# Kernel tuning notes

Measured on AMD Instinct MI355X. Metric: run time of the kernel, lower is better.

## Reference

```python
import jax, jax.numpy as jnp
import numpy as np

B, S, H = 8, 2048, 1024

def setup_inputs() -> dict:
    key = jax.random.key(0)
    k1, k2, k3, k4, k5, k6 = jax.random.split(key, 6)
    scale = 1.0 / np.sqrt(H)
    return {
        "hidden_states": jax.random.normal(k1, (B, S, H), dtype=jnp.float32),
        "key_padding_mask": jax.random.bernoulli(k2, 0.1, (B, S)),  # True = padded key
        "Wq_w": jax.random.normal(k3, (H, H), dtype=jnp.float32) * scale,
        "Wq_b": jax.random.normal(k4, (H,), dtype=jnp.float32) * 0.01,
        "Wk_w": jax.random.normal(k5, (H, H), dtype=jnp.float32) * scale,
        "Wk_b": jax.random.normal(k6, (H,), dtype=jnp.float32) * 0.01,
    }

def reference(hidden_states, key_padding_mask, Wq_w, Wq_b, Wk_w, Wk_b):
    # torch nn.Linear: y = x @ W.T + b
    q = jnp.einsum("bsh,oh->bso", hidden_states, Wq_w) + Wq_b
    k = jnp.einsum("bsh,oh->bso", hidden_states, Wk_w) + Wk_b
    d = q.shape[-1]
    scores = jnp.einsum("bqd,bkd->bqk", q, k) / jnp.sqrt(jnp.asarray(d, q.dtype))
    # scores[mask] -= inf  -> masked key columns become -inf
    scores = jnp.where(key_padding_mask[:, None, :], -jnp.inf, scores)
    attn = jax.nn.softmax(scores, axis=2)  # [B, S, S]
    out = jnp.einsum("bqk,bkd->bqd", attn, hidden_states)  # values = hidden_states (no proj)
    return out
```

## Files before the change

kernel.cpp:

```cpp
#include <hip/hip_runtime.h>
#include <hip/hip_bf16.h>

using bf16 = __hip_bfloat16;

using frag_ab = __attribute__((ext_vector_type(8))) short;
using frag_cd = __attribute__((ext_vector_type(4))) float;

__device__ __forceinline__ unsigned short f2bu(float f) {
    bf16 h = __float2bfloat16(f);
    return *(unsigned short*)&h;
}

__device__ __forceinline__ void st_c(float* p, float v) { *p = v; }
__device__ __forceinline__ void st_c(bf16* p, float v)  { *p = __float2bfloat16(v); }

__device__ __forceinline__ void load16(const bf16* g, bf16* l) {
    __builtin_amdgcn_global_load_lds(
        (const __attribute__((address_space(1))) unsigned int*)g,
        (__attribute__((address_space(3))) unsigned int*)l,
        16, 0, 0);
}

template <typename TC, bool HAS_BIAS, bool MASK>
__global__ __launch_bounds__(512, 2)
void gemm8p(const bf16* __restrict__ A, const bf16* __restrict__ B,
            const float* __restrict__ bias, const int* __restrict__ mask,
            TC* __restrict__ C, int K, int lda, int ldb, int ldc,
            long sA, long sB, long sC, long sM, float scale)
{
    __shared__ short lds[65536];

    const int bz = blockIdx.z;
    const bf16* Ab = A + (long)bz * sA;
    const bf16* Bb = B + (long)bz * sB;
    TC* Cb = C + (long)bz * sC;
    const int* maskb = MASK ? (mask + (long)bz * sM) : nullptr;

    const int t    = threadIdx.x;
    const int wid  = t >> 6;
    const int lane = t & 63;
    const int m0 = blockIdx.x * 256;
    const int n0 = blockIdx.y * 256;
    const int wr = wid >> 2;
    const int wc = wid & 3;
    const int lrow = lane & 15;
    const int quad = lane >> 4;

    const int rco   = ((quad + ((lrow >> 1) & 3)) & 3) * 8;
    const int a_off = wr * 4096 + lrow * 32 + rco;
    const int b_off = wc * 2048 + lrow * 32 + rco;

    const int srow = wid * 32 + (lane >> 2);
    const int gk   = (((lane & 3) - (lane >> 3)) & 3) * 8;
    const bf16* srcA0 = Ab + (long)(m0 + srow) * lda + gk;
    const bf16* srcA1 = Ab + (long)(m0 + srow + 16) * lda + gk;
    const bf16* srcB0 = Bb + (long)(n0 + srow) * ldb + gk;
    const bf16* srcB1 = Bb + (long)(n0 + srow + 16) * ldb + gk;
    const int dst0 = wid * 1024 + lane * 8;

    frag_cd acc[8][4] = {};
    frag_ab A0[4], A1[4], B0[4], B1[4];

#define STG(SLOT, PART, K0)                                                     \
    do {                                                                        \
        load16((PART ? srcB0 : srcA0) + (K0),                                   \
               (bf16*)&lds[(SLOT) * 16384 + (PART) * 8192 + dst0]);             \
        load16((PART ? srcB1 : srcA1) + (K0),                                   \
               (bf16*)&lds[(SLOT) * 16384 + (PART) * 8192 + dst0 + 512]);       \
    } while (0)

#define LOADA(DST, SLOT, QM)                                                    \
    do {                                                                        \
        _Pragma("unroll")                                                       \
        for (int i_ = 0; i_ < 4; ++i_)                                          \
            DST[i_] = *(const frag_ab*)&lds[(SLOT) * 16384 + a_off +            \
                                            (QM) * 2048 + i_ * 512];            \
    } while (0)

#define LOADB(DST, SLOT)                                                        \
    do {                                                                        \
        _Pragma("unroll")                                                       \
        for (int j_ = 0; j_ < 4; ++j_)                                          \
            DST[j_] = *(const frag_ab*)&lds[(SLOT) * 16384 + 8192 + b_off +     \
                                            j_ * 512];                          \
    } while (0)

#define MFMA16(AR, BR, QM)                                                      \
    do {                                                                        \
        _Pragma("unroll")                                                       \
        for (int i_ = 0; i_ < 4; ++i_)                                          \
            _Pragma("unroll")                                                   \
            for (int j_ = 0; j_ < 4; ++j_)                                      \
                acc[(QM) * 4 + i_][j_] = __builtin_amdgcn_mfma_f32_16x16x32_bf16( \
                    AR[i_], BR[j_], acc[(QM) * 4 + i_][j_], 0, 0, 0);           \
    } while (0)

#define VMW(N)                                                                  \
    do {                                                                        \
        if ((N) == 6)      asm volatile("s_waitcnt vmcnt(6)" ::: "memory");     \
        else if ((N) == 4) asm volatile("s_waitcnt vmcnt(4)" ::: "memory");     \
        else if ((N) == 0) asm volatile("s_waitcnt vmcnt(0)" ::: "memory");     \
    } while (0)

#define PH(AR, BR, QM, ISSUE, NSLOT, NAR, NBR, NQM, DO_STG, SSLOT, SPART, SK0, VMN) \
    do {                                                                        \
        if ((ISSUE) >= 1) LOADA(NAR, NSLOT, NQM);                               \
        if ((ISSUE) == 2) LOADB(NBR, NSLOT);                                    \
        if (DO_STG) STG(SSLOT, SPART, SK0);                                     \
        asm volatile("" ::: "memory");                                          \
        __builtin_amdgcn_s_setprio(1);                                          \
        MFMA16(AR, BR, QM);                                                     \
        __builtin_amdgcn_s_setprio(0);                                          \
        VMW(VMN);                                                               \
        asm volatile("" ::: "memory");                                          \
        __builtin_amdgcn_s_barrier();                                           \
        asm volatile("" ::: "memory");                                          \
    } while (0)

    STG(0, 0, 0);  STG(0, 1, 0);
    STG(1, 0, 32); STG(1, 1, 32);
    STG(2, 0, 64); STG(2, 1, 64);
    asm volatile("s_waitcnt vmcnt(8)" ::: "memory");
    __builtin_amdgcn_s_barrier();
    asm volatile("" ::: "memory");
    LOADA(A0, 0, 0);
    LOADB(B0, 0);

    const int NI = K >> 7;
    for (int it = 0; it < NI - 1; ++it) {
        const int kb = it << 7;
        PH(A0, B0, 0, 1, 0, A1, B1, 1, 1, 3, 0, kb + 96,   6);
        PH(A1, B0, 1, 2, 1, A0, B1, 0, 1, 3, 1, kb + 96,  -1);
        PH(A0, B1, 0, 1, 1, A1, B0, 1, 1, 0, 0, kb + 128,  6);
        PH(A1, B1, 1, 2, 2, A0, B0, 0, 1, 0, 1, kb + 128, -1);
        PH(A0, B0, 0, 1, 2, A1, B1, 1, 1, 1, 0, kb + 160,  6);
        PH(A1, B0, 1, 2, 3, A0, B1, 0, 1, 1, 1, kb + 160, -1);
        PH(A0, B1, 0, 1, 3, A1, B0, 1, 1, 2, 0, kb + 192,  6);
        PH(A1, B1, 1, 2, 0, A0, B0, 0, 1, 2, 1, kb + 192, -1);
    }
    {
        const int kb = (NI - 1) << 7;
        PH(A0, B0, 0, 1, 0, A1, B1, 1, 1, 3, 0, kb + 96,   6);
        PH(A1, B0, 1, 2, 1, A0, B1, 0, 1, 3, 1, kb + 96,  -1);
        PH(A0, B1, 0, 1, 1, A1, B0, 1, 0, 0, 0, 0,         4);
        PH(A1, B1, 1, 2, 2, A0, B0, 0, 0, 0, 0, 0,        -1);
        PH(A0, B0, 0, 1, 2, A1, B1, 1, 0, 0, 0, 0,         0);
        PH(A1, B0, 1, 2, 3, A0, B1, 0, 0, 0, 0, 0,        -1);
        PH(A0, B1, 0, 1, 3, A1, B0, 1, 0, 0, 0, 0,        -1);
        PH(A1, B1, 1, 0, 0, A0, B0, 0, 0, 0, 0, 0,        -1);
    }
#undef PH
#undef VMW
#undef MFMA16
#undef LOADB
#undef LOADA
#undef STG

#pragma unroll
    for (int j = 0; j < 4; ++j) {
        const int col = n0 + wc * 64 + j * 16 + lrow;
        const float bv = HAS_BIAS ? bias[col] : 0.0f;
        const bool msk = MASK ? (maskb[col] != 0) : false;
#pragma unroll
        for (int ai = 0; ai < 8; ++ai) {
            const int rbase = m0 + wr * 128 + ai * 16 + quad * 4;
#pragma unroll
            for (int r = 0; r < 4; ++r) {
                float v = acc[ai][j][r] * scale + bv;
                if (MASK && msk) v = -INFINITY;
                st_c(&Cb[(long)(rbase + r) * ldc + col], v);
            }
        }
    }
}

__global__ __launch_bounds__(256)
void convert_transpose(const float* __restrict__ X, bf16* __restrict__ Xb,
                       bf16* __restrict__ XT, int S, int H)
{
    __shared__ unsigned short tile[64][72];
    const int b = blockIdx.z;
    const float* Xp = X + (long)b * S * H;
    bf16* Xbp = Xb + (long)b * S * H;
    bf16* XTp = XT + (long)b * H * S;
    const int h0 = blockIdx.x * 64, s0 = blockIdx.y * 64;
    const int t = threadIdx.x;
    const int r  = t >> 4;
    const int c4 = (t & 15) * 4;

#pragma unroll
    for (int p = 0; p < 4; ++p) {
        const int row = r + p * 16;
        const float4 v = *(const float4*)&Xp[(long)(s0 + row) * H + h0 + c4];
        ushort4 u;
        u.x = f2bu(v.x); u.y = f2bu(v.y); u.z = f2bu(v.z); u.w = f2bu(v.w);
        *(ushort4*)&tile[row][c4] = u;
        *(ushort4*)&Xbp[(long)(s0 + row) * H + h0 + c4] = u;
    }
    __syncthreads();
#pragma unroll
    for (int p = 0; p < 4; ++p) {
        const int hrow = r + p * 16;
        ushort4 u;
        u.x = tile[c4 + 0][hrow];
        u.y = tile[c4 + 1][hrow];
        u.z = tile[c4 + 2][hrow];
        u.w = tile[c4 + 3][hrow];
        *(ushort4*)&XTp[(long)(h0 + hrow) * S + s0 + c4] = u;
    }
}

__global__ __launch_bounds__(256)
void convert_w2(const float* __restrict__ wa, const float* __restrict__ wb,
                bf16* __restrict__ out, int n4each)
{
    const int i = blockIdx.x * 256 + threadIdx.x;
    const bool second = i >= n4each;
    const float* src = second ? wb : wa;
    const int j = second ? i - n4each : i;
    const float4 v = ((const float4*)src)[j];
    ushort4 u;
    u.x = f2bu(v.x); u.y = f2bu(v.y); u.z = f2bu(v.z); u.w = f2bu(v.w);
    ((ushort4*)out)[i] = u;
}

__global__ __launch_bounds__(256)
void pack_bias(const float* __restrict__ qb, const float* __restrict__ kb,
               float* __restrict__ out, int H)
{
    const int i = blockIdx.x * 256 + threadIdx.x;
    out[i] = (i < H) ? qb[i] : kb[i - H];
}

__global__ __launch_bounds__(256)
void softmax_kernel(bf16* __restrict__ Smat, int Slen)
{
    const int row = blockIdx.x;
    bf16* srow = Smat + (long)row * Slen;

    const int t    = threadIdx.x;
    const int lane = t & 63;
    const int wid  = t >> 6;

    ushort4 u0 = ((const ushort4*)srow)[t * 2];
    ushort4 u1 = ((const ushort4*)srow)[t * 2 + 1];

    float vals[8];
    {
        const unsigned short us[8] = {u0.x, u0.y, u0.z, u0.w, u1.x, u1.y, u1.z, u1.w};
#pragma unroll
        for (int i = 0; i < 8; ++i) {
            unsigned int w = (unsigned int)us[i] << 16;
            vals[i] = *(float*)&w;
        }
    }

    float mx = vals[0];
#pragma unroll
    for (int i = 1; i < 8; ++i) mx = fmaxf(mx, vals[i]);

    __shared__ float red[4];
#pragma unroll
    for (int o = 32; o > 0; o >>= 1) mx = fmaxf(mx, __shfl_xor(mx, o, 64));
    if (lane == 0) red[wid] = mx;
    __syncthreads();
    mx = fmaxf(fmaxf(red[0], red[1]), fmaxf(red[2], red[3]));
    __syncthreads();

    float sum = 0.0f;
#pragma unroll
    for (int i = 0; i < 8; ++i) {
        const float e = __expf(vals[i] - mx);
        vals[i] = e;
        sum += e;
    }
#pragma unroll
    for (int o = 32; o > 0; o >>= 1) sum += __shfl_xor(sum, o, 64);
    if (lane == 0) red[wid] = sum;
    __syncthreads();
    sum = red[0] + red[1] + red[2] + red[3];

    const float inv = 1.0f / sum;
    ushort4 o0, o1;
    o0.x = f2bu(vals[0] * inv); o0.y = f2bu(vals[1] * inv);
    o0.z = f2bu(vals[2] * inv); o0.w = f2bu(vals[3] * inv);
    o1.x = f2bu(vals[4] * inv); o1.y = f2bu(vals[5] * inv);
    o1.z = f2bu(vals[6] * inv); o1.w = f2bu(vals[7] * inv);
    ((ushort4*)srow)[t * 2]     = o0;
    ((ushort4*)srow)[t * 2 + 1] = o1;
}

extern "C" void kernel_launch(void* const* d_in, const int* in_sizes, int n_in,
                              void* d_out, int out_size, void* d_ws, size_t ws_size,
                              hipStream_t stream)
{
    const float* hidden = (const float*)d_in[0];
    const int*   mask   = (const int*)d_in[1];
    const float* Wq_w   = (const float*)d_in[2];
    const float* Wq_b   = (const float*)d_in[3];
    const float* Wk_w   = (const float*)d_in[4];
    const float* Wk_b   = (const float*)d_in[5];
    float* out = (float*)d_out;

    const int B = 8, S = 2048, H = 1024;
    const int M = B * S;
    const long MH = (long)M * H;

    bf16* QK  = (bf16*)d_ws;
    bf16* XbT = QK + MH * 2;
    bf16* Sb  = XbT + MH;
    bf16* Xb  = Sb;
    bf16* Wb  = Xb + MH;
    float* biasP = (float*)(Wb + 2L * H * H);

    const dim3 blk(256);
    const dim3 blk512(512);

    convert_transpose<<<dim3(H / 64, S / 64, B), blk, 0, stream>>>(hidden, Xb, XbT, S, H);
    convert_w2<<<dim3(2 * H * H / 1024), blk, 0, stream>>>(Wq_w, Wk_w, Wb, H * H / 4);
    pack_bias<<<dim3(2 * H / 256), blk, 0, stream>>>(Wq_b, Wk_b, biasP, H);

    gemm8p<bf16, true, false><<<dim3(M / 256, 2 * H / 256, 1), blk512, 0, stream>>>(
        Xb, Wb, biasP, nullptr, QK, H, H, H, 2 * H, 0, 0, 0, 0, 1.0f);

    gemm8p<bf16, false, true><<<dim3(S / 256, S / 256, B), blk512, 0, stream>>>(
        QK, QK + H, nullptr, mask, Sb, H, 2 * H, 2 * H, S,
        (long)S * 2 * H, (long)S * 2 * H, (long)S * S, S, 1.0f / 32.0f);

    softmax_kernel<<<dim3(B * S), blk, 0, stream>>>(Sb, S);

    gemm8p<float, false, false><<<dim3(S / 256, H / 256, B), blk512, 0, stream>>>(
        Sb, XbT, nullptr, nullptr, out, S, S, S, H,
        (long)S * S, (long)H * S, (long)S * H, 0, 1.0f);
}
```

Measured before the change: 383.0 us.

## Fold Q and K projections into a single precomputed Wq^T Wk product

Uses the identity QK^T = X(Wq^T Wk)X^T + terms that are constant per row, which softmax cancels. The only term kept is a per-key bias X·(Wk^T bq), computed by a row-dot kernel. The combined weight matrix is built once per call by a small MFMA GEMM. This replaces the 2H-wide projection GEMM with one H-wide GEMM, and the scores GEMM now reads T and X directly. The cost is extra transposes and helper kernels, plus possible bf16 rounding differences from the reassociated product.

```diff
diff --git a/kernel.cpp b/kernel.cpp
--- a/kernel.cpp
+++ b/kernel.cpp
@@ -5,10 +5,18 @@
 
 using frag_ab = __attribute__((ext_vector_type(8))) short;
 using frag_cd = __attribute__((ext_vector_type(4))) float;
+
+#define TM 128
+#define TN 128
+#define TK 32
 
 __device__ __forceinline__ unsigned short f2bu(float f) {
     bf16 h = __float2bfloat16(f);
     return *(unsigned short*)&h;
+}
+__device__ __forceinline__ float bu2f(unsigned short u) {
+    unsigned int w = (unsigned int)u << 16;
+    return *(float*)&w;
 }
 
 __device__ __forceinline__ void st_c(float* p, float v) { *p = v; }
@@ -26,7 +34,7 @@
 void gemm8p(const bf16* __restrict__ A, const bf16* __restrict__ B,
             const float* __restrict__ bias, const int* __restrict__ mask,
             TC* __restrict__ C, int K, int lda, int ldb, int ldc,
-            long sA, long sB, long sC, long sM, float scale)
+            long sA, long sB, long sC, long sM, long sBias, float scale)
 {
     __shared__ short lds[65536];
 
@@ -35,6 +43,7 @@
     const bf16* Bb = B + (long)bz * sB;
     TC* Cb = C + (long)bz * sC;
     const int* maskb = MASK ? (mask + (long)bz * sM) : nullptr;
+    const float* biasb = HAS_BIAS ? (bias + (long)bz * sBias) : nullptr;
 
     const int t    = threadIdx.x;
     const int wid  = t >> 6;
@@ -159,14 +168,106 @@
 #pragma unroll
     for (int j = 0; j < 4; ++j) {
         const int col = n0 + wc * 64 + j * 16 + lrow;
+        const float bv = HAS_BIAS ? biasb[col] : 0.0f;
+        const bool msk = MASK ? (maskb[col] != 0) : false;
+#pragma unroll
+        for (int ai = 0; ai < 8; ++ai) {
+            const int rbase = m0 + wr * 128 + ai * 16 + quad * 4;
+#pragma unroll
+            for (int r = 0; r < 4; ++r) {
+                float v = acc[ai][j][r] * scale + bv;
+                if (MASK && msk) v = -INFINITY;
+                st_c(&Cb[(long)(rbase + r) * ldc + col], v);
+            }
+        }
+    }
+}
+
+template <typename TC, bool HAS_BIAS, bool MASK>
+__global__ __launch_bounds__(256, 4)
+void mfma_gemm_nt(const bf16* __restrict__ A, const bf16* __restrict__ B,
+                  const float* __restrict__ bias, const int* __restrict__ mask,
+                  TC* __restrict__ C, int N, int K, int lda, int ldb, int ldc,
+                  long sA, long sB, long sC, long sM, float scale)
+{
+    __shared__ bf16 As[2][TM][TK];
+    __shared__ bf16 Bs[2][TN][TK];
+
+    const int bz = blockIdx.z;
+    const bf16* Ab = A + (long)bz * sA;
+    const bf16* Bb = B + (long)bz * sB;
+    TC* Cb = C + (long)bz * sC;
+    const int* maskb = MASK ? (mask + (long)bz * sM) : nullptr;
+
+    const int t  = threadIdx.x;
+    const int m0 = blockIdx.x * TM;
+    const int n0 = blockIdx.y * TN;
+
+    const int srow = t >> 2;
+    const int c    = t & 3;
+    const int gco  = (((c - (srow >> 1)) & 3) << 3);
+    const int lco  = c << 3;
+    const bf16* ga0 = Ab + (long)(m0 + srow) * lda + gco;
+    const bf16* ga1 = ga0 + (long)64 * lda;
+    const bf16* gb0 = Bb + (long)(n0 + srow) * ldb + gco;
+    const bf16* gb1 = gb0 + (long)64 * ldb;
+
+    const int wave = t >> 6;
+    const int lane = t & 63;
+    const int wm   = (wave & 1) * 64;
+    const int wn   = (wave >> 1) * 64;
+    const int lrow = lane & 15;
+    const int quad = lane >> 4;
+    const int rco  = (((quad + (lrow >> 1)) & 3) << 3);
+
+    frag_cd acc[4][4] = {};
+
+#define STAGE(buf)                                         \
+    do {                                                   \
+        load16(ga0, &As[buf][srow][lco]);                  \
+        load16(ga1, &As[buf][srow + 64][lco]);             \
+        load16(gb0, &Bs[buf][srow][lco]);                  \
+        load16(gb1, &Bs[buf][srow + 64][lco]);             \
+        ga0 += TK; ga1 += TK; gb0 += TK; gb1 += TK;        \
+    } while (0)
+
+    STAGE(0);
+    __syncthreads();
+
+    int cur = 0;
+    for (int k0 = 0; k0 < K; k0 += TK) {
+        if (k0 + TK < K) STAGE(cur ^ 1);
+
+        frag_ab af[4], bfv[4];
+#pragma unroll
+        for (int i = 0; i < 4; ++i)
+            af[i] = *(const frag_ab*)&As[cur][wm + i * 16 + lrow][rco];
+#pragma unroll
+        for (int j = 0; j < 4; ++j)
+            bfv[j] = *(const frag_ab*)&Bs[cur][wn + j * 16 + lrow][rco];
+#pragma unroll
+        for (int i = 0; i < 4; ++i)
+#pragma unroll
+            for (int j = 0; j < 4; ++j)
+                acc[i][j] = __builtin_amdgcn_mfma_f32_16x16x32_bf16(
+                    af[i], bfv[j], acc[i][j], 0, 0, 0);
+
+        __syncthreads();
+        cur ^= 1;
+    }
+#undef STAGE
+
+#pragma unroll
+    for (int j = 0; j < 4; ++j) {
+        const int col = n0 + wn + j * 16 + lrow;
         const float bv = HAS_BIAS ? bias[col] : 0.0f;
         const bool msk = MASK ? (maskb[col] != 0) : false;
 #pragma unroll
-        for (int ai = 0; ai < 8; ++ai) {
-            const int rbase = m0 + wr * 128 + ai * 16 + quad * 4;
+        for (int i = 0; i < 4; ++i) {
+            const int rbase = m0 + wm + i * 16 + quad * 4;
 #pragma unroll
             for (int r = 0; r < 4; ++r) {
-                float v = acc[ai][j][r] * scale + bv;
+                float v = acc[i][j][r] * scale + bv;
                 if (MASK && msk) v = -INFINITY;
                 st_c(&Cb[(long)(rbase + r) * ldc + col], v);
             }
@@ -211,25 +312,25 @@
 }
 
 __global__ __launch_bounds__(256)
-void convert_w2(const float* __restrict__ wa, const float* __restrict__ wb,
-                bf16* __restrict__ out, int n4each)
-{
-    const int i = blockIdx.x * 256 + threadIdx.x;
-    const bool second = i >= n4each;
-    const float* src = second ? wb : wa;
-    const int j = second ? i - n4each : i;
-    const float4 v = ((const float4*)src)[j];
-    ushort4 u;
-    u.x = f2bu(v.x); u.y = f2bu(v.y); u.z = f2bu(v.z); u.w = f2bu(v.w);
-    ((ushort4*)out)[i] = u;
-}
-
-__global__ __launch_bounds__(256)
-void pack_bias(const float* __restrict__ qb, const float* __restrict__ kb,
-               float* __restrict__ out, int H)
-{
-    const int i = blockIdx.x * 256 + threadIdx.x;
-    out[i] = (i < H) ? qb[i] : kb[i - H];
+void rowdot1024(const bf16* __restrict__ A, const float* __restrict__ x,
+                float* __restrict__ y, float scale)
+{
+    const int wid  = threadIdx.x >> 6;
+    const int lane = threadIdx.x & 63;
+    const long row = (long)blockIdx.x * 4 + wid;
+    const bf16* a = A + row * 1024 + lane * 16;
+    const float* xp = x + lane * 16;
+
+    frag_ab u0 = *(const frag_ab*)a;
+    frag_ab u1 = *(const frag_ab*)(a + 8);
+    float s = 0.0f;
+#pragma unroll
+    for (int i = 0; i < 8; ++i) s += bu2f((unsigned short)u0[i]) * xp[i];
+#pragma unroll
+    for (int i = 0; i < 8; ++i) s += bu2f((unsigned short)u1[i]) * xp[i + 8];
+#pragma unroll
+    for (int o = 32; o > 0; o >>= 1) s += __shfl_xor(s, o, 64);
+    if (lane == 0) y[row] = s * scale;
 }
 
 __global__ __launch_bounds__(256)
@@ -249,10 +350,7 @@
     {
         const unsigned short us[8] = {u0.x, u0.y, u0.z, u0.w, u1.x, u1.y, u1.z, u1.w};
 #pragma unroll
-        for (int i = 0; i < 8; ++i) {
-            unsigned int w = (unsigned int)us[i] << 16;
-            vals[i] = *(float*)&w;
-        }
+        for (int i = 0; i < 8; ++i) vals[i] = bu2f(us[i]);
     }
 
     float mx = vals[0];
@@ -306,30 +404,40 @@
     const int M = B * S;
     const long MH = (long)M * H;
 
-    bf16* QK  = (bf16*)d_ws;
-    bf16* XbT = QK + MH * 2;
-    bf16* Sb  = XbT + MH;
-    bf16* Xb  = Sb;
-    bf16* Wb  = Xb + MH;
-    float* biasP = (float*)(Wb + 2L * H * H);
+    bf16* T   = (bf16*)d_ws;
+    bf16* XbT = T + MH;
+    bf16* Xb  = XbT + MH;
+    bf16* Sb  = Xb + MH;
+    bf16* WqT   = Sb;
+    bf16* WkT   = WqT + (long)H * H;
+    bf16* W2T   = WkT + (long)H * H;
+    bf16* dummy = W2T + (long)H * H;
+    float* wv   = (float*)(dummy + (long)H * H);
+    float* vbuf = (float*)d_out;
 
     const dim3 blk(256);
     const dim3 blk512(512);
 
     convert_transpose<<<dim3(H / 64, S / 64, B), blk, 0, stream>>>(hidden, Xb, XbT, S, H);
-    convert_w2<<<dim3(2 * H * H / 1024), blk, 0, stream>>>(Wq_w, Wk_w, Wb, H * H / 4);
-    pack_bias<<<dim3(2 * H / 256), blk, 0, stream>>>(Wq_b, Wk_b, biasP, H);
-
-    gemm8p<bf16, true, false><<<dim3(M / 256, 2 * H / 256, 1), blk512, 0, stream>>>(
-        Xb, Wb, biasP, nullptr, QK, H, H, H, 2 * H, 0, 0, 0, 0, 1.0f);
-
-    gemm8p<bf16, false, true><<<dim3(S / 256, S / 256, B), blk512, 0, stream>>>(
-        QK, QK + H, nullptr, mask, Sb, H, 2 * H, 2 * H, S,
-        (long)S * 2 * H, (long)S * 2 * H, (long)S * S, S, 1.0f / 32.0f);
+    convert_transpose<<<dim3(H / 64, H / 64, 1), blk, 0, stream>>>(Wq_w, dummy, WqT, H, H);
+    convert_transpose<<<dim3(H / 64, H / 64, 1), blk, 0, stream>>>(Wk_w, dummy, WkT, H, H);
+
+    rowdot1024<<<dim3(H / 4), blk, 0, stream>>>(WkT, Wq_b, wv, 1.0f);
+    rowdot1024<<<dim3(M / 4), blk, 0, stream>>>(Xb, wv, vbuf, 1.0f / 32.0f);
+
+    mfma_gemm_nt<bf16, false, false><<<dim3(H / TM, H / TN, 1), blk, 0, stream>>>(
+        WkT, WqT, nullptr, nullptr, W2T, H, H, H, H, H, 0, 0, 0, 0, 1.0f);
+
+    gemm8p<bf16, false, false><<<dim3(M / 256, H / 256, 1), blk512, 0, stream>>>(
+        Xb, W2T, nullptr, nullptr, T, H, H, H, H, 0, 0, 0, 0, 0, 1.0f);
+
+    gemm8p<bf16, true, true><<<dim3(S / 256, S / 256, B), blk512, 0, stream>>>(
+        T, Xb, vbuf, mask, Sb, H, H, H, S,
+        (long)S * H, (long)S * H, (long)S * S, S, S, 1.0f / 32.0f);
 
     softmax_kernel<<<dim3(B * S), blk, 0, stream>>>(Sb, S);
 
     gemm8p<float, false, false><<<dim3(S / 256, H / 256, B), blk512, 0, stream>>>(
         Sb, XbT, nullptr, nullptr, out, S, S, S, H,
-        (long)S * S, (long)H * S, (long)S * H, 0, 1.0f);
-}
+        (long)S * S, (long)H * S, (long)S * H, 0, 0, 1.0f);
+}
```

Result: no change. 386.2 us (+0.8%).

## Fuse softmax into score GEMM epilogue and row-normalize in PV GEMM

Applied to the files above, without the earlier changes.

The standalone softmax kernel is removed. The score GEMM now writes exp(score) directly, with masked keys set to zero. The PV GEMM accumulates row sums of the bf16 probabilities from its A fragments and divides the output by them in the epilogue. This saves a full read and write pass over the B×S×S score matrix and one kernel launch. The cost is dropping max-subtraction, so exp can overflow for large scores, plus extra ALU work inside the main MFMA loop.

```diff
diff --git a/kernel.cpp b/kernel.cpp
--- a/kernel.cpp
+++ b/kernel.cpp
@@ -9,6 +9,10 @@
 __device__ __forceinline__ unsigned short f2bu(float f) {
     bf16 h = __float2bfloat16(f);
     return *(unsigned short*)&h;
+}
+__device__ __forceinline__ float bu2f(unsigned short u) {
+    unsigned int w = (unsigned int)u << 16;
+    return *(float*)&w;
 }
 
 __device__ __forceinline__ void st_c(float* p, float v) { *p = v; }
@@ -21,7 +25,7 @@
         16, 0, 0);
 }
 
-template <typename TC, bool HAS_BIAS, bool MASK>
+template <typename TC, bool HAS_BIAS, bool MASK, bool EXPOUT, bool ROWDIV>
 __global__ __launch_bounds__(512, 2)
 void gemm8p(const bf16* __restrict__ A, const bf16* __restrict__ B,
             const float* __restrict__ bias, const int* __restrict__ mask,
@@ -60,6 +64,7 @@
 
     frag_cd acc[8][4] = {};
     frag_ab A0[4], A1[4], B0[4], B1[4];
+    float rs[8] = {};
 
 #define STG(SLOT, PART, K0)                                                     \
     do {                                                                        \
@@ -93,6 +98,22 @@
             for (int j_ = 0; j_ < 4; ++j_)                                      \
                 acc[(QM) * 4 + i_][j_] = __builtin_amdgcn_mfma_f32_16x16x32_bf16( \
                     AR[i_], BR[j_], acc[(QM) * 4 + i_][j_], 0, 0, 0);           \
+    } while (0)
+
+#define RSUM(AR, QM)                                                            \
+    do {                                                                        \
+        if constexpr (ROWDIV) {                                                 \
+            if (wc == 0) {                                                      \
+                _Pragma("unroll")                                               \
+                for (int i_ = 0; i_ < 4; ++i_) {                                \
+                    float s_ = 0.0f;                                            \
+                    _Pragma("unroll")                                           \
+                    for (int e_ = 0; e_ < 8; ++e_)                              \
+                        s_ += bu2f((unsigned short)AR[i_][e_]);                 \
+                    rs[(QM) * 4 + i_] += s_;                                    \
+                }                                                               \
+            }                                                                   \
+        }                                                                       \
     } while (0)
 
 #define VMW(N)                                                                  \
@@ -111,6 +132,7 @@
         __builtin_amdgcn_s_setprio(1);                                          \
         MFMA16(AR, BR, QM);                                                     \
         __builtin_amdgcn_s_setprio(0);                                          \
+        RSUM(AR, QM);                                                           \
         VMW(VMN);                                                               \
         asm volatile("" ::: "memory");                                          \
         __builtin_amdgcn_s_barrier();                                           \
@@ -151,11 +173,35 @@
     }
 #undef PH
 #undef VMW
+#undef RSUM
 #undef MFMA16
 #undef LOADB
 #undef LOADA
 #undef STG
 
+    float inv_l[8][4] = {};
+    if constexpr (ROWDIV) {
+        float* lshare = (float*)lds;
+#pragma unroll
+        for (int x_ = 0; x_ < 8; ++x_) {
+            float s_ = rs[x_];
+            s_ += __shfl_xor(s_, 16, 64);
+            s_ += __shfl_xor(s_, 32, 64);
+            rs[x_] = s_;
+        }
+        if (wc == 0 && quad == 0) {
+#pragma unroll
+            for (int x_ = 0; x_ < 8; ++x_)
+                lshare[wr * 128 + (x_ >> 2) * 64 + (x_ & 3) * 16 + lrow] = rs[x_];
+        }
+        __syncthreads();
+#pragma unroll
+        for (int ai = 0; ai < 8; ++ai)
+#pragma unroll
+            for (int r = 0; r < 4; ++r)
+                inv_l[ai][r] = 1.0f / lshare[wr * 128 + ai * 16 + quad * 4 + r];
+    }
+
 #pragma unroll
     for (int j = 0; j < 4; ++j) {
         const int col = n0 + wc * 64 + j * 16 + lrow;
@@ -167,7 +213,12 @@
 #pragma unroll
             for (int r = 0; r < 4; ++r) {
                 float v = acc[ai][j][r] * scale + bv;
-                if (MASK && msk) v = -INFINITY;
+                if constexpr (EXPOUT) {
+                    v = (MASK && msk) ? 0.0f : __expf(v);
+                } else {
+                    if (MASK && msk) v = -INFINITY;
+                    if constexpr (ROWDIV) v *= inv_l[ai][r];
+                }
                 st_c(&Cb[(long)(rbase + r) * ldc + col], v);
             }
         }
@@ -232,64 +283,6 @@
     out[i] = (i < H) ? qb[i] : kb[i - H];
 }
 
-__global__ __launch_bounds__(256)
-void softmax_kernel(bf16* __restrict__ Smat, int Slen)
-{
-    const int row = blockIdx.x;
-    bf16* srow = Smat + (long)row * Slen;
-
-    const int t    = threadIdx.x;
-    const int lane = t & 63;
-    const int wid  = t >> 6;
-
-    ushort4 u0 = ((const ushort4*)srow)[t * 2];
-    ushort4 u1 = ((const ushort4*)srow)[t * 2 + 1];
-
-    float vals[8];
-    {
-        const unsigned short us[8] = {u0.x, u0.y, u0.z, u0.w, u1.x, u1.y, u1.z, u1.w};
-#pragma unroll
-        for (int i = 0; i < 8; ++i) {
-            unsigned int w = (unsigned int)us[i] << 16;
-            vals[i] = *(float*)&w;
-        }
-    }
-
-    float mx = vals[0];
-#pragma unroll
-    for (int i = 1; i < 8; ++i) mx = fmaxf(mx, vals[i]);
-
-    __shared__ float red[4];
-#pragma unroll
-    for (int o = 32; o > 0; o >>= 1) mx = fmaxf(mx, __shfl_xor(mx, o, 64));
-    if (lane == 0) red[wid] = mx;
-    __syncthreads();
-    mx = fmaxf(fmaxf(red[0], red[1]), fmaxf(red[2], red[3]));
-    __syncthreads();
-
-    float sum = 0.0f;
-#pragma unroll
-    for (int i = 0; i < 8; ++i) {
-        const float e = __expf(vals[i] - mx);
-        vals[i] = e;
-        sum += e;
-    }
-#pragma unroll
-    for (int o = 32; o > 0; o >>= 1) sum += __shfl_xor(sum, o, 64);
-    if (lane == 0) red[wid] = sum;
-    __syncthreads();
-    sum = red[0] + red[1] + red[2] + red[3];
-
-    const float inv = 1.0f / sum;
-    ushort4 o0, o1;
-    o0.x = f2bu(vals[0] * inv); o0.y = f2bu(vals[1] * inv);
-    o0.z = f2bu(vals[2] * inv); o0.w = f2bu(vals[3] * inv);
-    o1.x = f2bu(vals[4] * inv); o1.y = f2bu(vals[5] * inv);
-    o1.z = f2bu(vals[6] * inv); o1.w = f2bu(vals[7] * inv);
-    ((ushort4*)srow)[t * 2]     = o0;
-    ((ushort4*)srow)[t * 2 + 1] = o1;
-}
-
 extern "C" void kernel_launch(void* const* d_in, const int* in_sizes, int n_in,
                               void* d_out, int out_size, void* d_ws, size_t ws_size,
                               hipStream_t stream)
@@ -320,16 +313,17 @@
     convert_w2<<<dim3(2 * H * H / 1024), blk, 0, stream>>>(Wq_w, Wk_w, Wb, H * H / 4);
     pack_bias<<<dim3(2 * H / 256), blk, 0, stream>>>(Wq_b, Wk_b, biasP, H);
 
-    gemm8p<bf16, true, false><<<dim3(M / 256, 2 * H / 256, 1), blk512, 0, stream>>>(
+    gemm8p<bf16, true, false, false, false>
+        <<<dim3(M / 256, 2 * H / 256, 1), blk512, 0, stream>>>(
         Xb, Wb, biasP, nullptr, QK, H, H, H, 2 * H, 0, 0, 0, 0, 1.0f);
 
-    gemm8p<bf16, false, true><<<dim3(S / 256, S / 256, B), blk512, 0, stream>>>(
+    gemm8p<bf16, false, true, true, false>
+        <<<dim3(S / 256, S / 256, B), blk512, 0, stream>>>(
         QK, QK + H, nullptr, mask, Sb, H, 2 * H, 2 * H, S,
         (long)S * 2 * H, (long)S * 2 * H, (long)S * S, S, 1.0f / 32.0f);
 
-    softmax_kernel<<<dim3(B * S), blk, 0, stream>>>(Sb, S);
-
-    gemm8p<float, false, false><<<dim3(S / 256, H / 256, B), blk512, 0, stream>>>(
+    gemm8p<float, false, false, false, true>
+        <<<dim3(S / 256, H / 256, B), blk512, 0, stream>>>(
         Sb, XbT, nullptr, nullptr, out, S, S, S, H,
         (long)S * S, (long)H * S, (long)S * H, 0, 1.0f);
 }
```

New measurement: 518.2 us. 1.35x slower.
